# Kernel tuning notes

Hardware: AMD Instinct MI355X
Metric: run time of the kernel (lower is better)

The kernel has to match this reference:

```python
import jax, jax.numpy as jnp
import numpy as np

N_EMB = 512
EMB_DIM = 64
BETA = 0.25


def setup_inputs() -> dict:
    key = jax.random.key(0)
    k1, k2 = jax.random.split(key)
    z = jax.random.normal(k1, (32, EMB_DIM, 64, 64), dtype=jnp.float32)
    # nn.Embedding weight init: uniform(-1/n_embeddings, 1/n_embeddings)
    codebook = jax.random.uniform(k2, (N_EMB, EMB_DIM), dtype=jnp.float32,
                                  minval=-1.0 / N_EMB, maxval=1.0 / N_EMB)
    return {"z": z, "codebook": codebook}


def reference(z, codebook):
    # z: [B, C, H, W] -> [B, H, W, C]
    z_nhwc = jnp.transpose(z, (0, 2, 3, 1))
    B, H, W, C = z_nhwc.shape
    zf = z_nhwc.reshape(-1, C)  # [N, C]
    # squared L2 distances to each code: ||z||^2 + ||e||^2 - 2 z.e
    dist = (jnp.sum(zf * zf, axis=1, keepdims=True)
            + jnp.sum(codebook * codebook, axis=1)
            - 2.0 * jnp.matmul(zf, codebook.T))  # [N, n_emb]
    indices = jnp.argmin(dist, axis=1)  # [N]
    # one-hot @ codebook == gather (same math, efficient form)
    z_q = codebook[indices].reshape(B, H, W, C)
    embedding_loss = jnp.mean((jax.lax.stop_gradient(z_q) - z_nhwc) ** 2)
    # straight-through estimator
    z_q_st = z_nhwc + jax.lax.stop_gradient(z_q - z_nhwc)
    z_q_out = jnp.transpose(z_q_st, (0, 3, 1, 2))  # back to [B, C, H, W]
    return (embedding_loss, z_q_out, indices)
```

## Files before the change

kernel.cpp:

```cpp
#include <hip/hip_runtime.h>


#define C_DIM   64
#define N_EMB   512
#define HW      4096
#define N_PIX   (32 * HW)
#define ZQ_OFF  1
#define IDX_OFF (1 + N_PIX * C_DIM)
#define NBLK    512

typedef _Float16 half8 __attribute__((ext_vector_type(8)));
typedef float    f32x4 __attribute__((ext_vector_type(4)));
union FragH { unsigned u[4]; half8 h8; uint4 u4; _Float16 h[8]; };

__device__ __forceinline__ unsigned umn(unsigned a, unsigned b){ return a<b?a:b; }
__device__ __forceinline__ unsigned umx(unsigned a, unsigned b){ return a>b?a:b; }

__global__ __launch_bounds__(512, 4) void vq_main(
    const float* __restrict__ z,
    const float* __restrict__ cb,
    float* __restrict__ out,
    float* __restrict__ ws)
{
    __shared__ unsigned cbh[N_EMB * 32];
    __shared__ float    esh5[N_EMB];
    __shared__ float    eshx[N_EMB];
    __shared__ float    wsum[8];

    const int t = threadIdx.x;

    {
        const float* e = cb + t * C_DIM;
        float ev[64];
        #pragma unroll
        for (int q = 0; q < 16; ++q) {
            float4 v = ((const float4*)e)[q];
            ev[4*q+0]=v.x; ev[4*q+1]=v.y; ev[4*q+2]=v.z; ev[4*q+3]=v.w;
        }
        float r[8];
        #pragma unroll
        for (int i = 0; i < 8; ++i) r[i] = __fmul_rn(ev[i], ev[i]);
        #pragma unroll
        for (int k = 8; k < 64; k += 8) {
            #pragma unroll
            for (int i = 0; i < 8; ++i)
                r[i] = __fadd_rn(r[i], __fmul_rn(ev[k+i], ev[k+i]));
        }
        float es = __fadd_rn(
            __fadd_rn(__fadd_rn(r[0],r[1]), __fadd_rn(r[2],r[3])),
            __fadd_rn(__fadd_rn(r[4],r[5]), __fadd_rn(r[6],r[7])));
        eshx[t] = es;
        esh5[t] = es + 0.5f;
        unsigned hw_[32];
        #pragma unroll
        for (int w2 = 0; w2 < 32; ++w2) {
            union { _Float16 h[2]; unsigned u; } pk;
            pk.h[0] = (_Float16)(ev[2*w2]   * 512.0f);
            pk.h[1] = (_Float16)(ev[2*w2+1] * 512.0f);
            hw_[w2] = pk.u;
        }
        const int rs = t & 7;
        #pragma unroll
        for (int g = 0; g < 8; ++g) {
            int g2 = g ^ rs;
            *(uint4*)&cbh[t*32 + g2*4] =
                make_uint4(hw_[4*g], hw_[4*g+1], hw_[4*g+2], hw_[4*g+3]);
        }
    }
    __syncthreads();

    const int l   = t & 63;
    const int wv  = t >> 6;
    const int lg  = l >> 4;
    const int li  = l & 15;
    const int bb  = blockIdx.x >> 4;
    const int g20 = (lg)     ^ (li & 7);
    const int g21 = (4 + lg) ^ (li & 7);
    const int jb  = lg * 4;
    float ls = 0.f;

    const int pxw0 = blockIdx.x * 256 + wv * 32;
    const float* zb0 = z + (size_t)bb * (C_DIM * HW) + ((pxw0      + li) & (HW-1));
    const float* zb1 = z + (size_t)bb * (C_DIM * HW) + ((pxw0 + 16 + li) & (HW-1));
    FragH bA0, bA1, bB0, bB1;
    {
        const float* c0 = zb0 + (size_t)(lg*8) * HW;
        const float* c1 = zb0 + (size_t)(32 + lg*8) * HW;
        const float* c2 = zb1 + (size_t)(lg*8) * HW;
        const float* c3 = zb1 + (size_t)(32 + lg*8) * HW;
        #pragma unroll
        for (int i = 0; i < 8; ++i) {
            bA0.h[i] = (_Float16)c0[(size_t)i*HW];
            bA1.h[i] = (_Float16)c1[(size_t)i*HW];
            bB0.h[i] = (_Float16)c2[(size_t)i*HW];
            bB1.h[i] = (_Float16)c3[(size_t)i*HW];
        }
    }

    unsigned k1A=0xFFFFFFFFu,k2A=0xFFFFFFFFu,k3A=0xFFFFFFFFu;
    unsigned k1B=0xFFFFFFFFu,k2B=0xFFFFFFFFu,k3B=0xFFFFFFFFu;
    #pragma unroll 4
    for (int T = 0; T < 32; ++T) {
        const int row = T*16 + li;
        FragH a0, a1;
        a0.u4 = *(const uint4*)&cbh[row*32 + g20*4];
        a1.u4 = *(const uint4*)&cbh[row*32 + g21*4];
        f32x4 es = *(const f32x4*)&esh5[T*16 + jb];
        f32x4 accA = {0.f,0.f,0.f,0.f}, accB = {0.f,0.f,0.f,0.f};
        accA = __builtin_amdgcn_mfma_f32_16x16x32_f16(a0.h8, bA0.h8, accA, 0,0,0);
        accA = __builtin_amdgcn_mfma_f32_16x16x32_f16(a1.h8, bA1.h8, accA, 0,0,0);
        accB = __builtin_amdgcn_mfma_f32_16x16x32_f16(a0.h8, bB0.h8, accB, 0,0,0);
        accB = __builtin_amdgcn_mfma_f32_16x16x32_f16(a1.h8, bB1.h8, accB, 0,0,0);
        const int jT = T*16 + jb;
        #pragma unroll
        for (int r2 = 0; r2 < 4; ++r2) {
            float dA = __fmaf_rn(-0.00390625f, accA[r2], es[r2]);
            float dB = __fmaf_rn(-0.00390625f, accB[r2], es[r2]);
            unsigned keyA = (__float_as_uint(dA) & 0xFFFFFE00u) | (unsigned)(jT + r2);
            unsigned keyB = (__float_as_uint(dB) & 0xFFFFFE00u) | (unsigned)(jT + r2);
            unsigned m1,M1,m2,M2;
            m1=umn(k1A,keyA); M1=umx(k1A,keyA); k1A=m1;
            m2=umn(k2A,M1);   M2=umx(k2A,M1);   k2A=m2; k3A=umn(k3A,M2);
            m1=umn(k1B,keyB); M1=umx(k1B,keyB); k1B=m1;
            m2=umn(k2B,M1);   M2=umx(k2B,M1);   k2B=m2; k3B=umn(k3B,M2);
        }
    }

    unsigned f1 = __shfl_xor(k1A, 32, 64), f2 = __shfl_xor(k2A, 32, 64), f3 = __shfl_xor(k3A, 32, 64);
    unsigned h1 = __shfl_xor(k1B, 32, 64), h2 = __shfl_xor(k2B, 32, 64), h3 = __shfl_xor(k3B, 32, 64);
    const bool isB = (l >= 32);
    unsigned c0 = isB ? k1B : k1A, c1 = isB ? k2B : k2A, c2 = isB ? k3B : k3A;
    unsigned c3 = isB ? h1  : f1,  c4 = isB ? h2  : f2,  c5 = isB ? h3  : f3;

    const float* zb = isB ? zb1 : zb0;
    const int px = pxw0 + (isB ? 16 : 0) + li;

    float zr[64];
    #pragma unroll
    for (int c = 0; c < 64; ++c) zr[c] = zb[(size_t)c * HW];
    float ap;
    {
        float r[8];
        #pragma unroll
        for (int i = 0; i < 8; ++i) r[i] = __fmul_rn(zr[i], zr[i]);
        #pragma unroll
        for (int k = 8; k < 64; k += 8) {
            #pragma unroll
            for (int i = 0; i < 8; ++i)
                r[i] = __fadd_rn(r[i], __fmul_rn(zr[k+i], zr[k+i]));
        }
        ap = __fadd_rn(
            __fadd_rn(__fadd_rn(r[0],r[1]), __fadd_rn(r[2],r[3])),
            __fadd_rn(__fadd_rn(r[4],r[5]), __fadd_rn(r[6],r[7])));
    }

    unsigned kmin = umn(umn(c0, c1), umn(umn(c2, c3), umn(c4, c5)));
    kmin = umn(kmin, __shfl_xor(kmin, 16, 64));
    const float thr = __uint_as_float(kmin & 0xFFFFFE00u) + 1.2e-4f;
    float bd = 3.0e38f; int bj = 1023;

    #define RESCORE(K) do {                                               \
        float da_ = __uint_as_float((K) & 0xFFFFFE00u);                   \
        if (da_ <= thr) {                                                 \
            int j_ = (int)((K) & 511u);                                   \
            const float* er_ = cb + (size_t)j_ * 64;                      \
            float a_ = 0.f;                                               \
            _Pragma("unroll")                                             \
            for (int c_ = 0; c_ < 64; ++c_)                               \
                a_ = __fmaf_rn(zr[c_], er_[c_], a_);                      \
            float dd_ = __fsub_rn(__fadd_rn(ap, eshx[j_]),                \
                                  __fmul_rn(2.0f, a_));                   \
            if (dd_ < bd || (dd_ == bd && j_ < bj)) { bd = dd_; bj = j_; }\
        }                                                                 \
    } while (0)
    RESCORE(c0); RESCORE(c1); RESCORE(c2);
    RESCORE(c3); RESCORE(c4); RESCORE(c5);
    #undef RESCORE

    {
        float od = __shfl_xor(bd, 16, 64);
        int   oj = __shfl_xor(bj, 16, 64);
        if (od < bd || (od == bd && oj < bj)) { bd = od; bj = oj; }
    }
    if ((l & 16) == 0) {
        out[IDX_OFF + px] = (float)bj;
        ls += bd;
    }

    {
        const int pm  = l & 31;
        const int hh  = l >> 5;
        const int src = (pm & 15) | ((pm & 16) << 1);
        const int bjw = __shfl(bj, src, 64);
        const float* eb = cb + (size_t)bjw * 64;
        float* zq = out + ZQ_OFF + (size_t)bb * (C_DIM * HW) + ((pxw0 + pm) & (HW-1));
        #pragma unroll
        for (int cc = 0; cc < 32; ++cc) {
            int c = hh * 32 + cc;
            zq[(size_t)c * HW] = eb[c];
        }
    }

    #pragma unroll
    for (int off = 32; off; off >>= 1) ls += __shfl_down(ls, off, 64);
    if (l == 0) wsum[wv] = ls;
    __syncthreads();
    if (t == 0) {
        float s = 0.f;
        #pragma unroll
        for (int i = 0; i < 8; ++i) s += wsum[i];
        ws[blockIdx.x] = s;
    }
}

__global__ __launch_bounds__(256) void vq_loss(
    const float* __restrict__ ws, float* __restrict__ out)
{
    __shared__ float sm[4];
    float v = ws[threadIdx.x] + ws[threadIdx.x + 256];
    #pragma unroll
    for (int off = 32; off; off >>= 1) v += __shfl_down(v, off, 64);
    const int lane = threadIdx.x & 63, wid = threadIdx.x >> 6;
    if (lane == 0) sm[wid] = v;
    __syncthreads();
    if (threadIdx.x == 0)
        out[0] = ((sm[0] + sm[1]) + (sm[2] + sm[3])) * (1.0f / 8388608.0f);
}

extern "C" void kernel_launch(void* const* d_in, const int* in_sizes, int n_in,
                              void* d_out, int out_size, void* d_ws, size_t ws_size,
                              hipStream_t stream)
{
    const float* z  = (const float*)d_in[0];
    const float* cb = (const float*)d_in[1];
    float* out = (float*)d_out;
    float* ws  = (float*)d_ws;

    vq_main<<<NBLK, 512, 0, stream>>>(z, cb, out, ws);
    vq_loss<<<1, 256, 0, stream>>>(ws, out);
}
```

Baseline: 43.22 us.

## Precompute fp16 codebook in a prep kernel and read it from global/L2

Moves codebook norm and fp16 packing out of every main block into a small prep kernel that writes a fragment-ordered layout to workspace. The main kernel then loads codebook fragments straight from global memory (L2-resident) instead of staging 64KB in LDS per block, and the grid changes to 1024 blocks of 256 threads. This drops the redundant per-block prologue and the LDS footprint, which should allow more resident blocks. In exchange the inner loop now issues global loads per tile and the pipeline needs an extra launch.

```diff
diff --git a/kernel.cpp b/kernel.cpp
--- a/kernel.cpp
+++ b/kernel.cpp
@@ -7,7 +7,10 @@
 #define N_PIX   (32 * HW)
 #define ZQ_OFF  1
 #define IDX_OFF (1 + N_PIX * C_DIM)
-#define NBLK    512
+#define NBLK    1024
+#define WS_ESH5 16384
+#define WS_ESHX 16896
+#define WS_LOSS 17408
 
 typedef _Float16 half8 __attribute__((ext_vector_type(8)));
 typedef float    f32x4 __attribute__((ext_vector_type(4)));
@@ -16,70 +19,68 @@
 __device__ __forceinline__ unsigned umn(unsigned a, unsigned b){ return a<b?a:b; }
 __device__ __forceinline__ unsigned umx(unsigned a, unsigned b){ return a>b?a:b; }
 
-__global__ __launch_bounds__(512, 4) void vq_main(
+__global__ __launch_bounds__(64) void vq_prep(
+    const float* __restrict__ cb, float* __restrict__ wsf)
+{
+    const int j = blockIdx.x * 64 + threadIdx.x;
+    const float* e = cb + j * C_DIM;
+    float ev[64];
+    #pragma unroll
+    for (int q = 0; q < 16; ++q) {
+        float4 v = ((const float4*)e)[q];
+        ev[4*q+0]=v.x; ev[4*q+1]=v.y; ev[4*q+2]=v.z; ev[4*q+3]=v.w;
+    }
+    float r[8];
+    #pragma unroll
+    for (int i = 0; i < 8; ++i) r[i] = __fmul_rn(ev[i], ev[i]);
+    #pragma unroll
+    for (int k = 8; k < 64; k += 8) {
+        #pragma unroll
+        for (int i = 0; i < 8; ++i)
+            r[i] = __fadd_rn(r[i], __fmul_rn(ev[k+i], ev[k+i]));
+    }
+    float es = __fadd_rn(
+        __fadd_rn(__fadd_rn(r[0],r[1]), __fadd_rn(r[2],r[3])),
+        __fadd_rn(__fadd_rn(r[4],r[5]), __fadd_rn(r[6],r[7])));
+    wsf[WS_ESHX + j] = es;
+    wsf[WS_ESH5 + j] = es + 0.5f;
+    unsigned hw_[32];
+    #pragma unroll
+    for (int w2 = 0; w2 < 32; ++w2) {
+        union { _Float16 h[2]; unsigned u; } pk;
+        pk.h[0] = (_Float16)(ev[2*w2]   * 512.0f);
+        pk.h[1] = (_Float16)(ev[2*w2+1] * 512.0f);
+        hw_[w2] = pk.u;
+    }
+    const int T = j >> 4, li = j & 15;
+    uint4* dst = (uint4*)wsf;
+    #pragma unroll
+    for (int g = 0; g < 8; ++g)
+        dst[(T*8 + g)*16 + li] =
+            make_uint4(hw_[4*g], hw_[4*g+1], hw_[4*g+2], hw_[4*g+3]);
+}
+
+__global__ __launch_bounds__(256, 4) void vq_main(
     const float* __restrict__ z,
     const float* __restrict__ cb,
     float* __restrict__ out,
-    float* __restrict__ ws)
-{
-    __shared__ unsigned cbh[N_EMB * 32];
-    __shared__ float    esh5[N_EMB];
-    __shared__ float    eshx[N_EMB];
-    __shared__ float    wsum[8];
-
-    const int t = threadIdx.x;
-
-    {
-        const float* e = cb + t * C_DIM;
-        float ev[64];
-        #pragma unroll
-        for (int q = 0; q < 16; ++q) {
-            float4 v = ((const float4*)e)[q];
-            ev[4*q+0]=v.x; ev[4*q+1]=v.y; ev[4*q+2]=v.z; ev[4*q+3]=v.w;
-        }
-        float r[8];
-        #pragma unroll
-        for (int i = 0; i < 8; ++i) r[i] = __fmul_rn(ev[i], ev[i]);
-        #pragma unroll
-        for (int k = 8; k < 64; k += 8) {
-            #pragma unroll
-            for (int i = 0; i < 8; ++i)
-                r[i] = __fadd_rn(r[i], __fmul_rn(ev[k+i], ev[k+i]));
-        }
-        float es = __fadd_rn(
-            __fadd_rn(__fadd_rn(r[0],r[1]), __fadd_rn(r[2],r[3])),
-            __fadd_rn(__fadd_rn(r[4],r[5]), __fadd_rn(r[6],r[7])));
-        eshx[t] = es;
-        esh5[t] = es + 0.5f;
-        unsigned hw_[32];
-        #pragma unroll
-        for (int w2 = 0; w2 < 32; ++w2) {
-            union { _Float16 h[2]; unsigned u; } pk;
-            pk.h[0] = (_Float16)(ev[2*w2]   * 512.0f);
-            pk.h[1] = (_Float16)(ev[2*w2+1] * 512.0f);
-            hw_[w2] = pk.u;
-        }
-        const int rs = t & 7;
-        #pragma unroll
-        for (int g = 0; g < 8; ++g) {
-            int g2 = g ^ rs;
-            *(uint4*)&cbh[t*32 + g2*4] =
-                make_uint4(hw_[4*g], hw_[4*g+1], hw_[4*g+2], hw_[4*g+3]);
-        }
-    }
-    __syncthreads();
-
+    float* __restrict__ wsf)
+{
+    __shared__ float wsum[4];
+
+    const int t   = threadIdx.x;
     const int l   = t & 63;
     const int wv  = t >> 6;
     const int lg  = l >> 4;
     const int li  = l & 15;
-    const int bb  = blockIdx.x >> 4;
-    const int g20 = (lg)     ^ (li & 7);
-    const int g21 = (4 + lg) ^ (li & 7);
-    const int jb  = lg * 4;
+    const int bb  = blockIdx.x >> 5;
     float ls = 0.f;
 
-    const int pxw0 = blockIdx.x * 256 + wv * 32;
+    const uint4* __restrict__ cbt  = (const uint4*)wsf;
+    const float* __restrict__ esh5 = wsf + WS_ESH5;
+    const float* __restrict__ eshx = wsf + WS_ESHX;
+
+    const int pxw0 = blockIdx.x * 128 + wv * 32;
     const float* zb0 = z + (size_t)bb * (C_DIM * HW) + ((pxw0      + li) & (HW-1));
     const float* zb1 = z + (size_t)bb * (C_DIM * HW) + ((pxw0 + 16 + li) & (HW-1));
     FragH bA0, bA1, bB0, bB1;
@@ -99,12 +100,12 @@
 
     unsigned k1A=0xFFFFFFFFu,k2A=0xFFFFFFFFu,k3A=0xFFFFFFFFu;
     unsigned k1B=0xFFFFFFFFu,k2B=0xFFFFFFFFu,k3B=0xFFFFFFFFu;
+    const int jb = lg * 4;
     #pragma unroll 4
     for (int T = 0; T < 32; ++T) {
-        const int row = T*16 + li;
         FragH a0, a1;
-        a0.u4 = *(const uint4*)&cbh[row*32 + g20*4];
-        a1.u4 = *(const uint4*)&cbh[row*32 + g21*4];
+        a0.u4 = cbt[(T*8 +     lg)*16 + li];
+        a1.u4 = cbt[(T*8 + 4 + lg)*16 + li];
         f32x4 es = *(const f32x4*)&esh5[T*16 + jb];
         f32x4 accA = {0.f,0.f,0.f,0.f}, accB = {0.f,0.f,0.f,0.f};
         accA = __builtin_amdgcn_mfma_f32_16x16x32_f16(a0.h8, bA0.h8, accA, 0,0,0);
@@ -205,19 +206,17 @@
     for (int off = 32; off; off >>= 1) ls += __shfl_down(ls, off, 64);
     if (l == 0) wsum[wv] = ls;
     __syncthreads();
-    if (t == 0) {
-        float s = 0.f;
-        #pragma unroll
-        for (int i = 0; i < 8; ++i) s += wsum[i];
-        ws[blockIdx.x] = s;
-    }
+    if (t == 0)
+        wsf[WS_LOSS + blockIdx.x] = (wsum[0] + wsum[1]) + (wsum[2] + wsum[3]);
 }
 
 __global__ __launch_bounds__(256) void vq_loss(
-    const float* __restrict__ ws, float* __restrict__ out)
+    const float* __restrict__ wsf, float* __restrict__ out)
 {
     __shared__ float sm[4];
-    float v = ws[threadIdx.x] + ws[threadIdx.x + 256];
+    const float* p = wsf + WS_LOSS;
+    float v = (p[threadIdx.x]       + p[threadIdx.x + 256])
+            + (p[threadIdx.x + 512] + p[threadIdx.x + 768]);
     #pragma unroll
     for (int off = 32; off; off >>= 1) v += __shfl_down(v, off, 64);
     const int lane = threadIdx.x & 63, wid = threadIdx.x >> 6;
@@ -234,8 +233,9 @@
     const float* z  = (const float*)d_in[0];
     const float* cb = (const float*)d_in[1];
     float* out = (float*)d_out;
-    float* ws  = (float*)d_ws;
-
-    vq_main<<<NBLK, 512, 0, stream>>>(z, cb, out, ws);
-    vq_loss<<<1, 256, 0, stream>>>(ws, out);
-}
+    float* wsf = (float*)d_ws;
+
+    vq_prep<<<8, 64, 0, stream>>>(cb, wsf);
+    vq_main<<<NBLK, 256, 0, stream>>>(z, cb, out, wsf);
+    vq_loss<<<1, 256, 0, stream>>>(wsf, out);
+}
```

Measured after the change: 47.71 us. 10.4% more time.
